# Performance work log

Hardware: AMD Instinct MI355X
Metric: run time of the kernel (lower is better)

## Reference

```python
import jax, jax.numpy as jnp
import numpy as np

EMB_DIM = 256
HEAD_DIM = 32


def setup_inputs() -> dict:
    key = jax.random.key(0)
    kx, kq, kk, kv = jax.random.split(key, 4)
    B, S = 4, 4096
    x = jax.random.normal(kx, (B, S, EMB_DIM), dtype=jnp.float32)
    # Linear(emb_dim, head_dim, bias=False): store as [emb_dim, head_dim]
    sc = 1.0 / np.sqrt(EMB_DIM)
    Wq = jax.random.normal(kq, (EMB_DIM, HEAD_DIM), dtype=jnp.float32) * sc
    Wk = jax.random.normal(kk, (EMB_DIM, HEAD_DIM), dtype=jnp.float32) * sc
    Wv = jax.random.normal(kv, (EMB_DIM, HEAD_DIM), dtype=jnp.float32) * sc
    return {"x": x, "Wq": Wq, "Wk": Wk, "Wv": Wv}


def reference(x, Wq, Wk, Wv):
    # single-head attention with POST-softmax scaling (as in source).
    # Dropout treated as identity (eval mode) for determinism.
    scaling = HEAD_DIM ** (-0.5)
    q = jnp.einsum('bse,ed->bsd', x, Wq)
    k = jnp.einsum('bse,ed->bsd', x, Wk)
    v = jnp.einsum('bse,ed->bsd', x, Wv)
    energy = jnp.einsum('bqd,bkd->bqk', q, k)  # [B,S,S]
    att = jax.nn.softmax(energy, axis=-1) * scaling
    out = jnp.einsum('bqk,bkd->bqd', att, v)
    return out
```

## Files before the change

kernel.cpp:

```cpp
#include <hip/hip_runtime.h>

#define EMB 256
#define HD 32
#define SEQ 4096
#define NSPLIT 8
#define KRANGE 512
#define NQROW 16384

typedef _Float16 half8 __attribute__((ext_vector_type(8)));
typedef _Float16 half4v __attribute__((ext_vector_type(4)));
typedef float floatx4 __attribute__((ext_vector_type(4)));
typedef float floatx16 __attribute__((ext_vector_type(16)));

#define L2E 1.44269504088896340736f
#define SCALING 0.17677669529663687f

__device__ __forceinline__ half8 mk8(unsigned a, unsigned b, unsigned c, unsigned d) {
  union { unsigned u[4]; half8 h; } z;
  z.u[0] = a; z.u[1] = b; z.u[2] = c; z.u[3] = d;
  return z.h;
}

__global__ __launch_bounds__(256) void prep_kernel(const float* __restrict__ Wq,
                                                   const float* __restrict__ Wk,
                                                   const float* __restrict__ Wv,
                                                   _Float16* __restrict__ wsw) {
  int gid = blockIdx.x * 256 + threadIdx.x;
  int j    = gid & 7;
  int lane = (gid >> 3) & 63;
  int kc   = (gid >> 9) & 7;
  int half = (gid >> 12) & 1;
  int mat  = gid >> 13;
  const float* W = (mat == 0) ? Wq : ((mat == 1) ? Wk : Wv);
  int n = lane & 15, quad = lane >> 4;
  int e = kc * 32 + quad * 8 + j;
  int d = n + half * 16;
  float v = W[e * HD + d];
  if (mat == 0) v *= L2E;
  wsw[gid] = (_Float16)v;
}

__global__ __launch_bounds__(256) void qkv_kernel(const float* __restrict__ x,
                                                  const _Float16* __restrict__ wsw,
                                                  _Float16* __restrict__ qw,
                                                  _Float16* __restrict__ kt2,
                                                  _Float16* __restrict__ vt2) {
  int lane = threadIdx.x & 63, wave = threadIdx.x >> 6;
  int n = lane & 15, quad = lane >> 4;
  int mat = blockIdx.y;
  int rowbase = blockIdx.x * 64 + wave * 16;

  floatx4 c0 = {0,0,0,0}, c1 = {0,0,0,0};

#pragma unroll
  for (int kc = 0; kc < 8; ++kc) {
    const float* xp = x + (rowbase + n) * EMB + kc * 32 + quad * 8;
    float4 xa = *(const float4*)(xp);
    float4 xb = *(const float4*)(xp + 4);
    half8 a;
    a[0] = (_Float16)xa.x; a[1] = (_Float16)xa.y; a[2] = (_Float16)xa.z; a[3] = (_Float16)xa.w;
    a[4] = (_Float16)xb.x; a[5] = (_Float16)xb.y; a[6] = (_Float16)xb.z; a[7] = (_Float16)xb.w;
    half8 b0 = *(const half8*)(wsw + (((mat * 2 + 0) * 8 + kc) << 9) + (lane << 3));
    half8 b1 = *(const half8*)(wsw + (((mat * 2 + 1) * 8 + kc) << 9) + (lane << 3));
    c0 = __builtin_amdgcn_mfma_f32_16x16x32_f16(a, b0, c0, 0, 0, 0);
    c1 = __builtin_amdgcn_mfma_f32_16x16x32_f16(a, b1, c1, 0, 0, 0);
  }

  if (mat == 0) {
#pragma unroll
    for (int r = 0; r < 4; ++r) {
      int row = rowbase + quad * 4 + r;
      qw[row * HD + n]      = (_Float16)c0[r];
      qw[row * HD + n + 16] = (_Float16)c1[r];
    }
  } else if (mat == 1) {
    int b = rowbase >> 12;
    int s0 = rowbase & (SEQ - 1);
    _Float16* kb2 = kt2 + (size_t)b * SEQ * HD;
    int hi = (n >> 3) << 5, j = n & 7;
#pragma unroll
    for (int r = 0; r < 4; ++r) {
      int s = s0 + quad * 4 + r;
      int tb = (s >> 5) << 10, n2k = s & 31;
      kb2[tb + ((n2k + hi) << 3) + j]       = (_Float16)c0[r];
      kb2[tb + 512 + ((n2k + hi) << 3) + j] = (_Float16)c1[r];
    }
  } else {
    int b = rowbase >> 12;
    int s0 = rowbase & (SEQ - 1);
    _Float16* vb = vt2 + (size_t)b * SEQ * HD;
#pragma unroll
    for (int r = 0; r < 4; ++r) {
      int s = s0 + quad * 4 + r;
      int blk = (s >> 3) << 8, sl = s & 7;
      vb[blk + n * 8 + sl]        = (_Float16)c0[r];
      vb[blk + (n + 16) * 8 + sl] = (_Float16)c1[r];
    }
  }
}

__global__ __launch_bounds__(256, 4) void attn_kernel(const _Float16* __restrict__ q,
                                                      const _Float16* __restrict__ kt2,
                                                      const _Float16* __restrict__ vt2,
                                                      _Float16* __restrict__ Op,
                                                      float* __restrict__ Mp,
                                                      float* __restrict__ Lp) {
  const int t = threadIdx.x;
  const int w = t >> 6, lane = t & 63;
  const int n2 = lane & 31, h = lane >> 5;
  const int qb = blockIdx.x & 127;
  const int sp = blockIdx.x >> 7;
  const int b = qb >> 5;
  const int qrow0 = qb * 128 + w * 32;
  const int key0 = sp * KRANGE;

  const _Float16* kb = kt2 + (size_t)(b * SEQ + key0) * HD;
  const _Float16* vb = vt2 + (size_t)(b * SEQ + key0) * HD;

  half8 qb0 = *(const half8*)(q + (qrow0 + n2) * HD + h * 8);
  half8 qb1 = *(const half8*)(q + (qrow0 + n2) * HD + 16 + h * 8);

  floatx16 o;
#pragma unroll
  for (int r = 0; r < 16; ++r) o[r] = 0.f;
  const floatx16 zero16 = o;
  float m = -__builtin_huge_valf();
  float l = 0.f;

  half8 ka0 = *(const half8*)(kb + lane * 8);
  half8 ka1 = *(const half8*)(kb + 512 + lane * 8);
  half8 va0 = *(const half8*)(vb + lane * 8);
  half8 va1 = *(const half8*)(vb + 512 + lane * 8);

#pragma unroll 2
  for (int kt = 0; kt < KRANGE / 32; ++kt) {
    half8 nka0, nka1, nva0, nva1;
    if (kt + 1 < KRANGE / 32) {
      const _Float16* kn = kb + (kt + 1) * 1024;
      const _Float16* vn = vb + (kt + 1) * 1024;
      nka0 = *(const half8*)(kn + lane * 8);
      nka1 = *(const half8*)(kn + 512 + lane * 8);
      nva0 = *(const half8*)(vn + lane * 8);
      nva1 = *(const half8*)(vn + 512 + lane * 8);
    }

    floatx16 s = __builtin_amdgcn_mfma_f32_32x32x16_f16(ka0, qb0, zero16, 0, 0, 0);
    s = __builtin_amdgcn_mfma_f32_32x32x16_f16(ka1, qb1, s, 0, 0, 0);

    floatx4 s0 = {s[0], s[1], s[2], s[3]};
    floatx4 s1 = {s[4], s[5], s[6], s[7]};
    floatx4 s2 = {s[8], s[9], s[10], s[11]};
    floatx4 s3 = {s[12], s[13], s[14], s[15]};
    floatx4 t01 = __builtin_elementwise_max(s0, s1);
    floatx4 t23 = __builtin_elementwise_max(s2, s3);
    floatx4 t4  = __builtin_elementwise_max(t01, t23);
    float mm = fmaxf(fmaxf(t4[0], t4[1]), fmaxf(t4[2], t4[3]));
    mm = fmaxf(mm, __shfl_xor(mm, 32));
    float mnew = fmaxf(m, mm);
    float alpha = __builtin_amdgcn_exp2f(m - mnew);
    m = mnew;

    float p[16];
#pragma unroll
    for (int r = 0; r < 16; ++r) p[r] = __builtin_amdgcn_exp2f(s[r] - mnew);
    unsigned pk[8];
#pragma unroll
    for (int g = 0; g < 8; ++g)
      pk[g] = __builtin_bit_cast(unsigned, __builtin_amdgcn_cvt_pkrtz(p[2 * g], p[2 * g + 1]));

    float ps = ((p[0] + p[1]) + (p[2] + p[3])) + ((p[4] + p[5]) + (p[6] + p[7]))
             + ((p[8] + p[9]) + (p[10] + p[11])) + ((p[12] + p[13]) + (p[14] + p[15]));
    ps += __shfl_xor(ps, 32);
    l = l * alpha + ps;

#pragma unroll
    for (int r = 0; r < 16; ++r) o[r] *= alpha;

    unsigned tmp0 = h ? pk[0] : pk[2];
    unsigned tmp1 = h ? pk[1] : pk[3];
    unsigned tmp2 = h ? pk[4] : pk[6];
    unsigned tmp3 = h ? pk[5] : pk[7];
    unsigned ex0 = (unsigned)__shfl_xor((int)tmp0, 32);
    unsigned ex1 = (unsigned)__shfl_xor((int)tmp1, 32);
    unsigned ex2 = (unsigned)__shfl_xor((int)tmp2, 32);
    unsigned ex3 = (unsigned)__shfl_xor((int)tmp3, 32);
    half8 B0 = h ? mk8(ex0, ex1, pk[2], pk[3]) : mk8(pk[0], pk[1], ex0, ex1);
    half8 B1 = h ? mk8(ex2, ex3, pk[6], pk[7]) : mk8(pk[4], pk[5], ex2, ex3);

    o = __builtin_amdgcn_mfma_f32_32x32x16_f16(va0, B0, o, 0, 0, 0);
    o = __builtin_amdgcn_mfma_f32_32x32x16_f16(va1, B1, o, 0, 0, 0);

    ka0 = nka0; ka1 = nka1; va0 = nva0; va1 = nva1;
  }

  size_t obase = ((size_t)(sp * NQROW + qrow0) + n2) * 32;
#pragma unroll
  for (int bb = 0; bb < 4; ++bb) {
    half4v pv;
    pv[0] = (_Float16)o[4 * bb + 0];
    pv[1] = (_Float16)o[4 * bb + 1];
    pv[2] = (_Float16)o[4 * bb + 2];
    pv[3] = (_Float16)o[4 * bb + 3];
    *(half4v*)&Op[obase + 8 * bb + 4 * h] = pv;
  }
  if (h == 0) {
    int mi = sp * NQROW + qrow0 + n2;
    Mp[mi] = m;
    Lp[mi] = l;
  }
}

__global__ __launch_bounds__(256) void combine_kernel(const _Float16* __restrict__ Op,
                                                      const float* __restrict__ Mp,
                                                      const float* __restrict__ Lp,
                                                      float* __restrict__ out) {
  int gid = blockIdx.x * 256 + threadIdx.x;
  int dc = gid & 7, qrow = gid >> 3;
  float mv[NSPLIT];
  float ms = -__builtin_huge_valf();
#pragma unroll
  for (int sp = 0; sp < NSPLIT; ++sp) {
    mv[sp] = Mp[sp * NQROW + qrow];
    ms = fmaxf(ms, mv[sp]);
  }
  float L = 0.f;
  floatx4 O = {0.f, 0.f, 0.f, 0.f};
#pragma unroll
  for (int sp = 0; sp < NSPLIT; ++sp) {
    float ww = __builtin_amdgcn_exp2f(mv[sp] - ms);
    L += ww * Lp[sp * NQROW + qrow];
    half4v ov = *(const half4v*)&Op[((size_t)(sp * NQROW + qrow)) * 32 + dc * 4];
#pragma unroll
    for (int r = 0; r < 4; ++r) O[r] += ww * (float)ov[r];
  }
  float inv = SCALING / L;
  floatx4 res = {O[0] * inv, O[1] * inv, O[2] * inv, O[3] * inv};
  *(floatx4*)&out[qrow * HD + dc * 4] = res;
}

extern "C" void kernel_launch(void* const* d_in, const int* in_sizes, int n_in,
                              void* d_out, int out_size, void* d_ws, size_t ws_size,
                              hipStream_t stream) {
  const float* x  = (const float*)d_in[0];
  const float* Wq = (const float*)d_in[1];
  const float* Wk = (const float*)d_in[2];
  const float* Wv = (const float*)d_in[3];
  float* out = (float*)d_out;

  _Float16* wsw = (_Float16*)d_ws;
  _Float16* qw  = wsw + 24576;
  _Float16* kt2 = qw + NQROW * HD;
  _Float16* vt2 = kt2 + NQROW * HD;
  _Float16* Op  = vt2 + NQROW * HD;
  float* Mp = (float*)(Op + (size_t)NSPLIT * NQROW * 32);
  float* Lp = Mp + NSPLIT * NQROW;

  prep_kernel<<<96, 256, 0, stream>>>(Wq, Wk, Wv, wsw);
  qkv_kernel<<<dim3(256, 3), 256, 0, stream>>>(x, wsw, qw, kt2, vt2);
  attn_kernel<<<1024, 256, 0, stream>>>(qw, kt2, vt2, Op, Mp, Lp);
  combine_kernel<<<512, 256, 0, stream>>>(Op, Mp, Lp, out);
}
```

Measured before the change: 100.6 us.

## Drop P shuffles via 32x32x8 PV MFMAs, lazy rescale, double key splits

The PV product now uses four 32x32x8 f16 MFMAs whose B operand is fed directly from the packed softmax probabilities. This removes the cross-lane shuffle exchange that rebuilt the 32x32x16 operand; V is loaded in a matching half4 layout instead. The alpha rescale of o and l now runs only when some lane's running max increases, decided with a wave ballot. The key range per block is halved and the split count doubled, giving twice as many attention blocks, at the price of more partial outputs for the combine kernel and, on gfx950, possibly lower MFMA throughput from the older 32x32x8 instruction.

Result: no change. 100.9 us (+0.3%).

```diff
diff --git a/kernel.cpp b/kernel.cpp
--- a/kernel.cpp
+++ b/kernel.cpp
@@ -3,8 +3,8 @@
 #define EMB 256
 #define HD 32
 #define SEQ 4096
-#define NSPLIT 8
-#define KRANGE 512
+#define NSPLIT 16
+#define KRANGE 256
 #define NQROW 16384
 
 typedef _Float16 half8 __attribute__((ext_vector_type(8)));
@@ -15,9 +15,9 @@
 #define L2E 1.44269504088896340736f
 #define SCALING 0.17677669529663687f
 
-__device__ __forceinline__ half8 mk8(unsigned a, unsigned b, unsigned c, unsigned d) {
-  union { unsigned u[4]; half8 h; } z;
-  z.u[0] = a; z.u[1] = b; z.u[2] = c; z.u[3] = d;
+__device__ __forceinline__ half4v mk4(unsigned a, unsigned b) {
+  union { unsigned u[2]; half4v h; } z;
+  z.u[0] = a; z.u[1] = b;
   return z.h;
 }
 
@@ -127,21 +127,27 @@
   float m = -__builtin_huge_valf();
   float l = 0.f;
 
+  const int voff = n2 * 8 + 4 * h;
   half8 ka0 = *(const half8*)(kb + lane * 8);
   half8 ka1 = *(const half8*)(kb + 512 + lane * 8);
-  half8 va0 = *(const half8*)(vb + lane * 8);
-  half8 va1 = *(const half8*)(vb + 512 + lane * 8);
+  half4v v0g = *(const half4v*)(vb + voff);
+  half4v v1g = *(const half4v*)(vb + 256 + voff);
+  half4v v2g = *(const half4v*)(vb + 512 + voff);
+  half4v v3g = *(const half4v*)(vb + 768 + voff);
 
 #pragma unroll 2
   for (int kt = 0; kt < KRANGE / 32; ++kt) {
-    half8 nka0, nka1, nva0, nva1;
+    half8 nka0, nka1;
+    half4v nv0, nv1, nv2, nv3;
     if (kt + 1 < KRANGE / 32) {
       const _Float16* kn = kb + (kt + 1) * 1024;
       const _Float16* vn = vb + (kt + 1) * 1024;
       nka0 = *(const half8*)(kn + lane * 8);
       nka1 = *(const half8*)(kn + 512 + lane * 8);
-      nva0 = *(const half8*)(vn + lane * 8);
-      nva1 = *(const half8*)(vn + 512 + lane * 8);
+      nv0 = *(const half4v*)(vn + voff);
+      nv1 = *(const half4v*)(vn + 256 + voff);
+      nv2 = *(const half4v*)(vn + 512 + voff);
+      nv3 = *(const half4v*)(vn + 768 + voff);
     }
 
     floatx16 s = __builtin_amdgcn_mfma_f32_32x32x16_f16(ka0, qb0, zero16, 0, 0, 0);
@@ -157,7 +163,13 @@
     float mm = fmaxf(fmaxf(t4[0], t4[1]), fmaxf(t4[2], t4[3]));
     mm = fmaxf(mm, __shfl_xor(mm, 32));
     float mnew = fmaxf(m, mm);
-    float alpha = __builtin_amdgcn_exp2f(m - mnew);
+
+    if (__ballot(mm > m) != 0ULL) {
+      float alpha = __builtin_amdgcn_exp2f(m - mnew);
+      l *= alpha;
+#pragma unroll
+      for (int r = 0; r < 16; ++r) o[r] *= alpha;
+    }
     m = mnew;
 
     float p[16];
@@ -171,26 +183,15 @@
     float ps = ((p[0] + p[1]) + (p[2] + p[3])) + ((p[4] + p[5]) + (p[6] + p[7]))
              + ((p[8] + p[9]) + (p[10] + p[11])) + ((p[12] + p[13]) + (p[14] + p[15]));
     ps += __shfl_xor(ps, 32);
-    l = l * alpha + ps;
-
-#pragma unroll
-    for (int r = 0; r < 16; ++r) o[r] *= alpha;
-
-    unsigned tmp0 = h ? pk[0] : pk[2];
-    unsigned tmp1 = h ? pk[1] : pk[3];
-    unsigned tmp2 = h ? pk[4] : pk[6];
-    unsigned tmp3 = h ? pk[5] : pk[7];
-    unsigned ex0 = (unsigned)__shfl_xor((int)tmp0, 32);
-    unsigned ex1 = (unsigned)__shfl_xor((int)tmp1, 32);
-    unsigned ex2 = (unsigned)__shfl_xor((int)tmp2, 32);
-    unsigned ex3 = (unsigned)__shfl_xor((int)tmp3, 32);
-    half8 B0 = h ? mk8(ex0, ex1, pk[2], pk[3]) : mk8(pk[0], pk[1], ex0, ex1);
-    half8 B1 = h ? mk8(ex2, ex3, pk[6], pk[7]) : mk8(pk[4], pk[5], ex2, ex3);
-
-    o = __builtin_amdgcn_mfma_f32_32x32x16_f16(va0, B0, o, 0, 0, 0);
-    o = __builtin_amdgcn_mfma_f32_32x32x16_f16(va1, B1, o, 0, 0, 0);
-
-    ka0 = nka0; ka1 = nka1; va0 = nva0; va1 = nva1;
+    l += ps;
+
+    o = __builtin_amdgcn_mfma_f32_32x32x8f16(v0g, mk4(pk[0], pk[1]), o, 0, 0, 0);
+    o = __builtin_amdgcn_mfma_f32_32x32x8f16(v1g, mk4(pk[2], pk[3]), o, 0, 0, 0);
+    o = __builtin_amdgcn_mfma_f32_32x32x8f16(v2g, mk4(pk[4], pk[5]), o, 0, 0, 0);
+    o = __builtin_amdgcn_mfma_f32_32x32x8f16(v3g, mk4(pk[6], pk[7]), o, 0, 0, 0);
+
+    ka0 = nka0; ka1 = nka1;
+    v0g = nv0; v1g = nv1; v2g = nv2; v3g = nv3;
   }
 
   size_t obase = ((size_t)(sp * NQROW + qrow0) + n2) * 32;
@@ -257,6 +258,6 @@
 
   prep_kernel<<<96, 256, 0, stream>>>(Wq, Wk, Wv, wsw);
   qkv_kernel<<<dim3(256, 3), 256, 0, stream>>>(x, wsw, qw, kt2, vt2);
-  attn_kernel<<<1024, 256, 0, stream>>>(qw, kt2, vt2, Op, Mp, Lp);
+  attn_kernel<<<2048, 256, 0, stream>>>(qw, kt2, vt2, Op, Mp, Lp);
   combine_kernel<<<512, 256, 0, stream>>>(Op, Mp, Lp, out);
 }
```
